# Performance work log

Measured on AMD Instinct MI355X. Metric: run time of the kernel, lower is better.

The kernel has to match this reference:

```python
import jax, jax.numpy as jnp
import numpy as np

B, T, C = 2, 2048, 1024
N_HEAD = 16
BAND_WIDTH = 256

def setup_inputs() -> dict:
    key = jax.random.key(0)
    ks = jax.random.split(key, 5)
    s = 1.0 / np.sqrt(C)
    return {
        "x": jax.random.normal(ks[0], (B, T, C), dtype=jnp.float32),
        "Wq": jax.random.normal(ks[1], (C, C), dtype=jnp.float32) * s,
        "bq": jnp.zeros((C,), dtype=jnp.float32),
        "Wk": jax.random.normal(ks[2], (C, C), dtype=jnp.float32) * s,
        "bk": jnp.zeros((C,), dtype=jnp.float32),
        "Wv": jax.random.normal(ks[3], (C, C), dtype=jnp.float32) * s,
        "bv": jnp.zeros((C,), dtype=jnp.float32),
        "Wp": jax.random.normal(ks[4], (C, C), dtype=jnp.float32) * s,
        "bp": jnp.zeros((C,), dtype=jnp.float32),
    }

def _band_mask(t):
    # allowed: j <= i (causal) and j >= i - band_width (band)
    i = jnp.arange(t)[:, None]
    j = jnp.arange(t)[None, :]
    return (j <= i) & (j >= i - BAND_WIDTH)

def reference(x, Wq, bq, Wk, bk, Wv, bv, Wp, bp):
    b, t, c = x.shape
    hd = c // N_HEAD
    # projections -> [b, h, t, hd]
    def heads(w, bias):
        y = x @ w.T + bias
        return y.reshape(b, t, N_HEAD, hd).transpose(0, 2, 1, 3)
    q = heads(Wq, bq)
    k = heads(Wk, bk)
    v = heads(Wv, bv)
    scale = 1.0 / np.sqrt(hd)
    att = jnp.einsum('bhqd,bhkd->bhqk', q, k) * scale  # [b,h,t,t]
    mask = _band_mask(t)
    att = jnp.where(mask[None, None], att, -jnp.inf)
    att = jax.nn.softmax(att, axis=-1)
    y = jnp.einsum('bhqk,bhkd->bhqd', att, v)
    y = y.transpose(0, 2, 1, 3).reshape(b, t, c)
    return y @ Wp.T + bp
```

## Files before the change

### kernel.cpp

```cpp
#include <hip/hip_runtime.h>


typedef __attribute__((ext_vector_type(8))) short bf16x8;
typedef __attribute__((ext_vector_type(8))) unsigned short u16x8;
typedef __attribute__((ext_vector_type(4))) float f32x4;

__device__ __forceinline__ float bf2f(unsigned short u) {
  union { unsigned u; float f; } x; x.u = ((unsigned)u) << 16; return x.f;
}
__device__ __forceinline__ unsigned short f2bf(float f) {
  union { float f; unsigned u; } x; x.f = f;
  unsigned r = x.u + 0x7FFFu + ((x.u >> 16) & 1u);
  return (unsigned short)(r >> 16);
}

#define GLOAD_LDS16(g, l)                                                     \
  __builtin_amdgcn_global_load_lds(                                           \
      (__attribute__((address_space(1))) void*)(g),                           \
      (__attribute__((address_space(3))) void*)(l), 16, 0, 0)

__global__ void cvt_all(const float* __restrict__ x, const float* __restrict__ Wq,
                        const float* __restrict__ Wk, const float* __restrict__ Wv,
                        const float* __restrict__ Wp, unsigned short* __restrict__ xb,
                        unsigned short* __restrict__ wqkv,
                        unsigned short* __restrict__ wpb) {
  int i = blockIdx.x * 256 + threadIdx.x;
  const float* src;
  unsigned short* dst;
  int off;
  if (i < 1048576)      { src = x;  dst = xb;             off = i; }
  else if (i < 1310720) { src = Wq; dst = wqkv;           off = i - 1048576; }
  else if (i < 1572864) { src = Wk; dst = wqkv + 1048576; off = i - 1310720; }
  else if (i < 1835008) { src = Wv; dst = wqkv + 2097152; off = i - 1572864; }
  else                  { src = Wp; dst = wpb;            off = i - 1835008; }
  float4 v = ((const float4*)src)[off];
  ushort4 o;
  o.x = f2bf(v.x); o.y = f2bf(v.y); o.z = f2bf(v.z); o.w = f2bf(v.w);
  ((ushort4*)dst)[off] = o;
}

template <int MODE>
__global__ __launch_bounds__(256) void gemm_bt(
    const unsigned short* __restrict__ A, const unsigned short* __restrict__ Wall,
    const float* __restrict__ b0, const float* __restrict__ b1,
    const float* __restrict__ b2, void* __restrict__ outp) {
  constexpr int K = 1024;
  __shared__ __align__(16) unsigned short As[128 * 32];
  __shared__ __align__(16) unsigned short Bs[128 * 32];
  int tid = threadIdx.x;
  int m0 = blockIdx.x * 128;
  int n0;
  const unsigned short* W;
  const float* bias;
  void* out;
  int proj = 0;
  if (MODE == 1) {
    proj = blockIdx.y >> 3;
    n0 = (blockIdx.y & 7) * 128;
    W = Wall + (size_t)proj * (K * 1024);
    bias = (proj == 0) ? b0 : ((proj == 1) ? b1 : b2);
    out = (void*)((unsigned short*)outp + (size_t)proj * 4194304);
  } else {
    n0 = blockIdx.y * 128;
    W = Wall;
    bias = b0;
    out = outp;
  }
  int w = tid >> 6, lane = tid & 63;
  int wm = (w >> 1) * 64, wn = (w & 1) * 64;
  int lm = lane & 15, quad = lane >> 4;

  f32x4 acc[4][4];
#pragma unroll
  for (int mi = 0; mi < 4; ++mi)
#pragma unroll
    for (int ni = 0; ni < 4; ++ni) acc[mi][ni] = (f32x4){0.f, 0.f, 0.f, 0.f};

  int o0 = tid * 16, o1 = o0 + 4096;
  int r0 = o0 >> 6, cb0 = o0 & 63;
  int r1 = o1 >> 6, cb1 = o1 & 63;
  const char* a0 = (const char*)A + (size_t)(m0 + r0) * (K * 2) + cb0;
  const char* a1 = (const char*)A + (size_t)(m0 + r1) * (K * 2) + cb1;
  const char* w0 = (const char*)W + (size_t)(n0 + r0) * (K * 2) + cb0;
  const char* w1 = (const char*)W + (size_t)(n0 + r1) * (K * 2) + cb1;
  char* lA = (char*)As;
  char* lB = (char*)Bs;

  for (int k0 = 0; k0 < K; k0 += 32) {
    GLOAD_LDS16(a0 + k0 * 2, lA + o0);
    GLOAD_LDS16(a1 + k0 * 2, lA + o1);
    GLOAD_LDS16(w0 + k0 * 2, lB + o0);
    GLOAD_LDS16(w1 + k0 * 2, lB + o1);
    __syncthreads();
    bf16x8 af[4], bfv[4];
#pragma unroll
    for (int mi = 0; mi < 4; ++mi)
      af[mi] = *(const bf16x8*)(As + (wm + mi * 16 + lm) * 32 + quad * 8);
#pragma unroll
    for (int ni = 0; ni < 4; ++ni)
      bfv[ni] = *(const bf16x8*)(Bs + (wn + ni * 16 + lm) * 32 + quad * 8);
#pragma unroll
    for (int mi = 0; mi < 4; ++mi)
#pragma unroll
      for (int ni = 0; ni < 4; ++ni)
        acc[mi][ni] = __builtin_amdgcn_mfma_f32_16x16x32_bf16(
            af[mi], bfv[ni], acc[mi][ni], 0, 0, 0);
    __syncthreads();
  }
#pragma unroll
  for (int mi = 0; mi < 4; ++mi) {
#pragma unroll
    for (int ni = 0; ni < 4; ++ni) {
      int gn = n0 + wn + ni * 16 + lm;
      float bv = bias[gn];
#pragma unroll
      for (int r = 0; r < 4; ++r) {
        int gm = m0 + wm + mi * 16 + quad * 4 + r;
        float val = acc[mi][ni][r] + bv;
        if (MODE == 0) {
          ((float*)out)[(size_t)gm * 1024 + gn] = val;
        } else {
          int bb = gm >> 11, tt = gm & 2047;
          int hh = gn >> 6, dd = gn & 63;
          size_t idx;
          if (proj == 2)
            idx = (((size_t)bb * 16 + hh) * 64 + dd) * 2048 + tt;
          else
            idx = (((size_t)bb * 16 + hh) * 2048 + tt) * 64 + dd;
          ((unsigned short*)out)[idx] = f2bf(val);
        }
      }
    }
  }
}

__global__ __launch_bounds__(256) void attn_band_mfma(
    const unsigned short* __restrict__ qb, const unsigned short* __restrict__ kb,
    const unsigned short* __restrict__ vtg, unsigned short* __restrict__ yb) {
  __shared__ __align__(16) unsigned short Kb[64 * 72];
  __shared__ __align__(16) unsigned short Vb[64 * 72];
  __shared__ __align__(16) unsigned short Ps[64 * 72];
  int bid = blockIdx.x;
  int qt = bid & 31, h = (bid >> 5) & 15, b = bid >> 9;
  int q0b = qt * 64;
  int tid = threadIdx.x;
  int lane = tid & 63;
  int w = tid >> 6;
  int m = lane & 15, quad = lane >> 4;
  int wq = w * 16;
  int tq0 = q0b + wq;
  size_t hb = ((size_t)(b * 16 + h)) * (2048 * 64);
  size_t vhb = ((size_t)(b * 16 + h)) * (64 * 2048);
  const char* kgb = (const char*)(kb + hb);
  const char* vgb = (const char*)(vtg + vhb);

  int sA = tid, sB = tid + 256, sC = 512 + (tid & 63);
  int rA = sA / 9, kA = sA - rA * 9;
  int rB = sB / 9, kB = sB - rB * 9;
  int rC = sC / 9, kC = sC - rC * 9;
  int okA = (kA < 8) ? kA : 0, okB = (kB < 8) ? kB : 0, okC = (kC < 8) ? kC : 0;
  int offKA = rA * 128 + okA * 16, offVA = rA * 4096 + okA * 16;
  int offKB = rB * 128 + okB * 16, offVB = rB * 4096 + okB * 16;
  int offKC = rC * 128 + okC * 16, offVC = rC * 4096 + okC * 16;
  char* KbB = (char*)Kb;
  char* VbB = (char*)Vb;

  const unsigned short* qrow = qb + hb + (size_t)(tq0 + m) * 64;
  bf16x8 af0 = *(const bf16x8*)(qrow + quad * 8);
  bf16x8 af1 = *(const bf16x8*)(qrow + 32 + quad * 8);

  f32x4 oacc[4];
#pragma unroll
  for (int di = 0; di < 4; ++di) oacc[di] = (f32x4){0.f, 0.f, 0.f, 0.f};
  float lpart[4] = {0.f, 0.f, 0.f, 0.f};

  int jlo = q0b - 256;
  if (jlo < 0) jlo = 0;
  for (int c0 = jlo; c0 <= q0b; c0 += 64) {
    const char* kg = kgb + (size_t)c0 * 128;
    const char* vg = vgb + (size_t)c0 * 2;
    __syncthreads();
    GLOAD_LDS16(kg + offKA, KbB + sA * 16);
    GLOAD_LDS16(kg + offKB, KbB + sB * 16);
    GLOAD_LDS16(vg + offVA, VbB + sA * 16);
    GLOAD_LDS16(vg + offVB, VbB + sB * 16);
    if (tid < 128) {
      const char* g = (tid < 64) ? (kg + offKC) : (vg + offVC);
      char* l = ((tid < 64) ? KbB : VbB) + sC * 16;
      GLOAD_LDS16(g, l);
    }
    __syncthreads();

    f32x4 sacc[4];
#pragma unroll
    for (int ni = 0; ni < 4; ++ni) sacc[ni] = (f32x4){0.f, 0.f, 0.f, 0.f};
#pragma unroll
    for (int ni = 0; ni < 4; ++ni) {
      bf16x8 k0 = *(const bf16x8*)(Kb + (ni * 16 + m) * 72 + quad * 8);
      bf16x8 k1 = *(const bf16x8*)(Kb + (ni * 16 + m) * 72 + 32 + quad * 8);
      sacc[ni] = __builtin_amdgcn_mfma_f32_16x16x32_bf16(af0, k0, sacc[ni], 0, 0, 0);
      sacc[ni] = __builtin_amdgcn_mfma_f32_16x16x32_bf16(af1, k1, sacc[ni], 0, 0, 0);
    }
#pragma unroll
    for (int ni = 0; ni < 4; ++ni) {
      int j = c0 + ni * 16 + m;
#pragma unroll
      for (int r = 0; r < 4; ++r) {
        int t = tq0 + quad * 4 + r;
        float e = __expf(sacc[ni][r] * 0.125f);
        e = ((unsigned)(t - j) <= 256u) ? e : 0.f;
        lpart[r] += e;
        Ps[(wq + quad * 4 + r) * 72 + ni * 16 + m] = f2bf(e);
      }
    }
#pragma unroll
    for (int ks = 0; ks < 2; ++ks) {
      bf16x8 a = *(const bf16x8*)(Ps + (wq + m) * 72 + ks * 32 + quad * 8);
#pragma unroll
      for (int di = 0; di < 4; ++di) {
        bf16x8 vfr = *(const bf16x8*)(Vb + (di * 16 + m) * 72 + ks * 32 + quad * 8);
        oacc[di] = __builtin_amdgcn_mfma_f32_16x16x32_bf16(a, vfr, oacc[di], 0, 0, 0);
      }
    }
  }
#pragma unroll
  for (int mask = 1; mask <= 8; mask <<= 1)
#pragma unroll
    for (int r = 0; r < 4; ++r) lpart[r] += __shfl_xor(lpart[r], mask, 64);
  float inv[4];
#pragma unroll
  for (int r = 0; r < 4; ++r) inv[r] = 1.f / lpart[r];
#pragma unroll
  for (int di = 0; di < 4; ++di)
#pragma unroll
    for (int r = 0; r < 4; ++r)
      Ps[(wq + quad * 4 + r) * 72 + di * 16 + m] = f2bf(oacc[di][r] * inv[r]);
  size_t orow = (size_t)b * 2048 + tq0;
#pragma unroll
  for (int v2 = 0; v2 < 2; ++v2) {
    int v = v2 * 64 + lane;
    int q = v >> 3, dg = v & 7;
    u16x8 val = *(const u16x8*)(Ps + (wq + q) * 72 + dg * 8);
    *(u16x8*)(yb + (orow + q) * 1024 + h * 64 + dg * 8) = val;
  }
}

extern "C" void kernel_launch(void* const* d_in, const int* in_sizes, int n_in,
                              void* d_out, int out_size, void* d_ws,
                              size_t ws_size, hipStream_t stream) {
  const float* x  = (const float*)d_in[0];
  const float* Wq = (const float*)d_in[1];
  const float* bq = (const float*)d_in[2];
  const float* Wk = (const float*)d_in[3];
  const float* bk = (const float*)d_in[4];
  const float* Wv = (const float*)d_in[5];
  const float* bv = (const float*)d_in[6];
  const float* Wp = (const float*)d_in[7];
  const float* bp = (const float*)d_in[8];
  float* out = (float*)d_out;

  char* ws = (char*)d_ws;
  unsigned short* xb   = (unsigned short*)(ws);
  unsigned short* wqkv = (unsigned short*)(ws + (8ull << 20));
  unsigned short* wpb  = (unsigned short*)(ws + (14ull << 20));
  unsigned short* qkv  = (unsigned short*)(ws + (16ull << 20));
  unsigned short* yb   = (unsigned short*)(ws + (40ull << 20));

  cvt_all<<<8192, 256, 0, stream>>>(x, Wq, Wk, Wv, Wp, xb, wqkv, wpb);
  gemm_bt<1><<<dim3(32, 24), 256, 0, stream>>>(xb, wqkv, bq, bk, bv, (void*)qkv);
  attn_band_mfma<<<1024, 256, 0, stream>>>(qkv, qkv + 4194304ull,
                                           qkv + 8388608ull, yb);
  gemm_bt<0><<<dim3(32, 8), 256, 0, stream>>>(yb, wpb, bp, nullptr, nullptr,
                                              (void*)out);
}
```

Before: 169.9 us.

## Double-buffer K/V tiles in band attention and use 64-row tiles for output projection

```diff
diff --git a/kernel.cpp b/kernel.cpp
--- a/kernel.cpp
+++ b/kernel.cpp
@@ -39,33 +39,20 @@
   ((ushort4*)dst)[off] = o;
 }
 
-template <int MODE>
-__global__ __launch_bounds__(256) void gemm_bt(
+__global__ __launch_bounds__(256) void gemm_qkv(
     const unsigned short* __restrict__ A, const unsigned short* __restrict__ Wall,
     const float* __restrict__ b0, const float* __restrict__ b1,
-    const float* __restrict__ b2, void* __restrict__ outp) {
+    const float* __restrict__ b2, unsigned short* __restrict__ outp) {
   constexpr int K = 1024;
   __shared__ __align__(16) unsigned short As[128 * 32];
   __shared__ __align__(16) unsigned short Bs[128 * 32];
   int tid = threadIdx.x;
   int m0 = blockIdx.x * 128;
-  int n0;
-  const unsigned short* W;
-  const float* bias;
-  void* out;
-  int proj = 0;
-  if (MODE == 1) {
-    proj = blockIdx.y >> 3;
-    n0 = (blockIdx.y & 7) * 128;
-    W = Wall + (size_t)proj * (K * 1024);
-    bias = (proj == 0) ? b0 : ((proj == 1) ? b1 : b2);
-    out = (void*)((unsigned short*)outp + (size_t)proj * 4194304);
-  } else {
-    n0 = blockIdx.y * 128;
-    W = Wall;
-    bias = b0;
-    out = outp;
-  }
+  int proj = blockIdx.y >> 3;
+  int n0 = (blockIdx.y & 7) * 128;
+  const unsigned short* W = Wall + (size_t)proj * (K * 1024);
+  const float* bias = (proj == 0) ? b0 : ((proj == 1) ? b1 : b2);
+  unsigned short* out = outp + (size_t)proj * 4194304;
   int w = tid >> 6, lane = tid & 63;
   int wm = (w >> 1) * 64, wn = (w & 1) * 64;
   int lm = lane & 15, quad = lane >> 4;
@@ -117,18 +104,76 @@
       for (int r = 0; r < 4; ++r) {
         int gm = m0 + wm + mi * 16 + quad * 4 + r;
         float val = acc[mi][ni][r] + bv;
-        if (MODE == 0) {
-          ((float*)out)[(size_t)gm * 1024 + gn] = val;
-        } else {
-          int bb = gm >> 11, tt = gm & 2047;
-          int hh = gn >> 6, dd = gn & 63;
-          size_t idx;
-          if (proj == 2)
-            idx = (((size_t)bb * 16 + hh) * 64 + dd) * 2048 + tt;
-          else
-            idx = (((size_t)bb * 16 + hh) * 2048 + tt) * 64 + dd;
-          ((unsigned short*)out)[idx] = f2bf(val);
-        }
+        int bb = gm >> 11, tt = gm & 2047;
+        int hh = gn >> 6, dd = gn & 63;
+        size_t idx;
+        if (proj == 2)
+          idx = (((size_t)bb * 16 + hh) * 64 + dd) * 2048 + tt;
+        else
+          idx = (((size_t)bb * 16 + hh) * 2048 + tt) * 64 + dd;
+        out[idx] = f2bf(val);
+      }
+    }
+  }
+}
+
+__global__ __launch_bounds__(256) void gemm_p64(
+    const unsigned short* __restrict__ A, const unsigned short* __restrict__ W,
+    const float* __restrict__ bias, float* __restrict__ out) {
+  constexpr int K = 1024;
+  __shared__ __align__(16) unsigned short As[64 * 32];
+  __shared__ __align__(16) unsigned short Bs[128 * 32];
+  int tid = threadIdx.x;
+  int m0 = blockIdx.x * 64, n0 = blockIdx.y * 128;
+  int w = tid >> 6, lane = tid & 63;
+  int wm = (w >> 1) * 32, wn = (w & 1) * 64;
+  int lm = lane & 15, quad = lane >> 4;
+
+  f32x4 acc[2][4];
+#pragma unroll
+  for (int mi = 0; mi < 2; ++mi)
+#pragma unroll
+    for (int ni = 0; ni < 4; ++ni) acc[mi][ni] = (f32x4){0.f, 0.f, 0.f, 0.f};
+
+  int o0 = tid * 16, o1 = o0 + 4096;
+  int r0 = o0 >> 6, cb0 = o0 & 63;
+  int r1 = o1 >> 6, cb1 = o1 & 63;
+  const char* ag = (const char*)A + (size_t)(m0 + r0) * (K * 2) + cb0;
+  const char* w0 = (const char*)W + (size_t)(n0 + r0) * (K * 2) + cb0;
+  const char* w1 = (const char*)W + (size_t)(n0 + r1) * (K * 2) + cb1;
+  char* lA = (char*)As;
+  char* lB = (char*)Bs;
+
+  for (int k0 = 0; k0 < K; k0 += 32) {
+    GLOAD_LDS16(ag + k0 * 2, lA + o0);
+    GLOAD_LDS16(w0 + k0 * 2, lB + o0);
+    GLOAD_LDS16(w1 + k0 * 2, lB + o1);
+    __syncthreads();
+    bf16x8 af[2], bfv[4];
+#pragma unroll
+    for (int mi = 0; mi < 2; ++mi)
+      af[mi] = *(const bf16x8*)(As + (wm + mi * 16 + lm) * 32 + quad * 8);
+#pragma unroll
+    for (int ni = 0; ni < 4; ++ni)
+      bfv[ni] = *(const bf16x8*)(Bs + (wn + ni * 16 + lm) * 32 + quad * 8);
+#pragma unroll
+    for (int mi = 0; mi < 2; ++mi)
+#pragma unroll
+      for (int ni = 0; ni < 4; ++ni)
+        acc[mi][ni] = __builtin_amdgcn_mfma_f32_16x16x32_bf16(
+            af[mi], bfv[ni], acc[mi][ni], 0, 0, 0);
+    __syncthreads();
+  }
+#pragma unroll
+  for (int mi = 0; mi < 2; ++mi) {
+#pragma unroll
+    for (int ni = 0; ni < 4; ++ni) {
+      int gn = n0 + wn + ni * 16 + lm;
+      float bv = bias[gn];
+#pragma unroll
+      for (int r = 0; r < 4; ++r) {
+        int gm = m0 + wm + mi * 16 + quad * 4 + r;
+        out[(size_t)gm * 1024 + gn] = acc[mi][ni][r] + bv;
       }
     }
   }
@@ -137,9 +182,8 @@
 __global__ __launch_bounds__(256) void attn_band_mfma(
     const unsigned short* __restrict__ qb, const unsigned short* __restrict__ kb,
     const unsigned short* __restrict__ vtg, unsigned short* __restrict__ yb) {
-  __shared__ __align__(16) unsigned short Kb[64 * 72];
-  __shared__ __align__(16) unsigned short Vb[64 * 72];
-  __shared__ __align__(16) unsigned short Ps[64 * 72];
+  __shared__ __align__(16) unsigned short Kb[2][64 * 72];
+  __shared__ __align__(16) unsigned short Vb[2][64 * 72];
   int bid = blockIdx.x;
   int qt = bid & 31, h = (bid >> 5) & 15, b = bid >> 9;
   int q0b = qt * 64;
@@ -162,8 +206,25 @@
   int offKA = rA * 128 + okA * 16, offVA = rA * 4096 + okA * 16;
   int offKB = rB * 128 + okB * 16, offVB = rB * 4096 + okB * 16;
   int offKC = rC * 128 + okC * 16, offVC = rC * 4096 + okC * 16;
-  char* KbB = (char*)Kb;
-  char* VbB = (char*)Vb;
+
+  int jlo = q0b - 256;
+  if (jlo < 0) jlo = 0;
+
+  {
+    const char* kg = kgb + (size_t)jlo * 128;
+    const char* vg = vgb + (size_t)jlo * 2;
+    char* kd = (char*)Kb[0];
+    char* vd = (char*)Vb[0];
+    GLOAD_LDS16(kg + offKA, kd + sA * 16);
+    GLOAD_LDS16(kg + offKB, kd + sB * 16);
+    GLOAD_LDS16(vg + offVA, vd + sA * 16);
+    GLOAD_LDS16(vg + offVB, vd + sB * 16);
+    if (tid < 128) {
+      const char* g = (tid < 64) ? (kg + offKC) : (vg + offVC);
+      char* l = ((tid < 64) ? kd : vd) + sC * 16;
+      GLOAD_LDS16(g, l);
+    }
+  }
 
   const unsigned short* qrow = qb + hb + (size_t)(tq0 + m) * 64;
   bf16x8 af0 = *(const bf16x8*)(qrow + quad * 8);
@@ -174,33 +235,38 @@
   for (int di = 0; di < 4; ++di) oacc[di] = (f32x4){0.f, 0.f, 0.f, 0.f};
   float lpart[4] = {0.f, 0.f, 0.f, 0.f};
 
-  int jlo = q0b - 256;
-  if (jlo < 0) jlo = 0;
-  for (int c0 = jlo; c0 <= q0b; c0 += 64) {
-    const char* kg = kgb + (size_t)c0 * 128;
-    const char* vg = vgb + (size_t)c0 * 2;
-    __syncthreads();
-    GLOAD_LDS16(kg + offKA, KbB + sA * 16);
-    GLOAD_LDS16(kg + offKB, KbB + sB * 16);
-    GLOAD_LDS16(vg + offVA, VbB + sA * 16);
-    GLOAD_LDS16(vg + offVB, VbB + sB * 16);
-    if (tid < 128) {
-      const char* g = (tid < 64) ? (kg + offKC) : (vg + offVC);
-      char* l = ((tid < 64) ? KbB : VbB) + sC * 16;
-      GLOAD_LDS16(g, l);
-    }
-    __syncthreads();
-
+  int cur = 0;
+  for (int c0 = jlo; c0 <= q0b; c0 += 64, cur ^= 1) {
+    __syncthreads();
+    const unsigned short* Kc = Kb[cur];
+    const unsigned short* Vc = Vb[cur];
     f32x4 sacc[4];
 #pragma unroll
     for (int ni = 0; ni < 4; ++ni) sacc[ni] = (f32x4){0.f, 0.f, 0.f, 0.f};
 #pragma unroll
     for (int ni = 0; ni < 4; ++ni) {
-      bf16x8 k0 = *(const bf16x8*)(Kb + (ni * 16 + m) * 72 + quad * 8);
-      bf16x8 k1 = *(const bf16x8*)(Kb + (ni * 16 + m) * 72 + 32 + quad * 8);
+      bf16x8 k0 = *(const bf16x8*)(Kc + (ni * 16 + m) * 72 + quad * 8);
+      bf16x8 k1 = *(const bf16x8*)(Kc + (ni * 16 + m) * 72 + 32 + quad * 8);
       sacc[ni] = __builtin_amdgcn_mfma_f32_16x16x32_bf16(af0, k0, sacc[ni], 0, 0, 0);
       sacc[ni] = __builtin_amdgcn_mfma_f32_16x16x32_bf16(af1, k1, sacc[ni], 0, 0, 0);
     }
+    __syncthreads();
+    if (c0 < q0b) {
+      const char* kg = kgb + (size_t)(c0 + 64) * 128;
+      const char* vg = vgb + (size_t)(c0 + 64) * 2;
+      char* kd = (char*)Kb[cur ^ 1];
+      char* vd = (char*)Vb[cur ^ 1];
+      GLOAD_LDS16(kg + offKA, kd + sA * 16);
+      GLOAD_LDS16(kg + offKB, kd + sB * 16);
+      GLOAD_LDS16(vg + offVA, vd + sA * 16);
+      GLOAD_LDS16(vg + offVB, vd + sB * 16);
+      if (tid < 128) {
+        const char* g = (tid < 64) ? (kg + offKC) : (vg + offVC);
+        char* l = ((tid < 64) ? kd : vd) + sC * 16;
+        GLOAD_LDS16(g, l);
+      }
+    }
+    unsigned short* Pw = (unsigned short*)Kc;
 #pragma unroll
     for (int ni = 0; ni < 4; ++ni) {
       int j = c0 + ni * 16 + m;
@@ -210,15 +276,15 @@
         float e = __expf(sacc[ni][r] * 0.125f);
         e = ((unsigned)(t - j) <= 256u) ? e : 0.f;
         lpart[r] += e;
-        Ps[(wq + quad * 4 + r) * 72 + ni * 16 + m] = f2bf(e);
+        Pw[(wq + quad * 4 + r) * 72 + ni * 16 + m] = f2bf(e);
       }
     }
 #pragma unroll
     for (int ks = 0; ks < 2; ++ks) {
-      bf16x8 a = *(const bf16x8*)(Ps + (wq + m) * 72 + ks * 32 + quad * 8);
+      bf16x8 a = *(const bf16x8*)(Pw + (wq + m) * 72 + ks * 32 + quad * 8);
 #pragma unroll
       for (int di = 0; di < 4; ++di) {
-        bf16x8 vfr = *(const bf16x8*)(Vb + (di * 16 + m) * 72 + ks * 32 + quad * 8);
+        bf16x8 vfr = *(const bf16x8*)(Vc + (di * 16 + m) * 72 + ks * 32 + quad * 8);
         oacc[di] = __builtin_amdgcn_mfma_f32_16x16x32_bf16(a, vfr, oacc[di], 0, 0, 0);
       }
     }
@@ -230,17 +296,18 @@
   float inv[4];
 #pragma unroll
   for (int r = 0; r < 4; ++r) inv[r] = 1.f / lpart[r];
+  unsigned short* R = &Kb[0][0];
 #pragma unroll
   for (int di = 0; di < 4; ++di)
 #pragma unroll
     for (int r = 0; r < 4; ++r)
-      Ps[(wq + quad * 4 + r) * 72 + di * 16 + m] = f2bf(oacc[di][r] * inv[r]);
+      R[(wq + quad * 4 + r) * 72 + di * 16 + m] = f2bf(oacc[di][r] * inv[r]);
   size_t orow = (size_t)b * 2048 + tq0;
 #pragma unroll
   for (int v2 = 0; v2 < 2; ++v2) {
     int v = v2 * 64 + lane;
     int q = v >> 3, dg = v & 7;
-    u16x8 val = *(const u16x8*)(Ps + (wq + q) * 72 + dg * 8);
+    u16x8 val = *(const u16x8*)(R + (wq + q) * 72 + dg * 8);
     *(u16x8*)(yb + (orow + q) * 1024 + h * 64 + dg * 8) = val;
   }
 }
@@ -267,9 +334,8 @@
   unsigned short* yb   = (unsigned short*)(ws + (40ull << 20));
 
   cvt_all<<<8192, 256, 0, stream>>>(x, Wq, Wk, Wv, Wp, xb, wqkv, wpb);
-  gemm_bt<1><<<dim3(32, 24), 256, 0, stream>>>(xb, wqkv, bq, bk, bv, (void*)qkv);
+  gemm_qkv<<<dim3(32, 24), 256, 0, stream>>>(xb, wqkv, bq, bk, bv, qkv);
   attn_band_mfma<<<1024, 256, 0, stream>>>(qkv, qkv + 4194304ull,
                                            qkv + 8388608ull, yb);
-  gemm_bt<0><<<dim3(32, 8), 256, 0, stream>>>(yb, wpb, bp, nullptr, nullptr,
-                                              (void*)out);
-}
+  gemm_p64<<<dim3(64, 8), 256, 0, stream>>>(yb, wpb, bp, out);
+}
```

Measured after the change: 166.7 us. Within noise of the previous version (-1.9%).
